# Kernel tuning notes

Hardware: AMD Instinct MI355X
Metric: run time of the kernel (lower is better)

Reference implementation:

```python
import jax, jax.numpy as jnp
import numpy as np

HEADS = 8

def _ape(f, c):
    # sinusoidal positional encoding, matches PositionalEncoding buffer pe[:f]
    pos = jnp.arange(f, dtype=jnp.float32)[:, None]                      # [f,1]
    div = jnp.exp(jnp.arange(0, c, 2, dtype=jnp.float32) * (-np.log(10000.0) / c))  # [c/2]
    pe = jnp.zeros((f, c), dtype=jnp.float32)
    pe = pe.at[:, 0::2].set(jnp.sin(pos * div))
    pe = pe.at[:, 1::2].set(jnp.cos(pos * div))
    return pe


def setup_inputs() -> dict:
    key = jax.random.key(0)
    ks = jax.random.split(key, 6)
    b, f, d, c = 2, 16, 4096, 320
    s = 1.0 / np.sqrt(c)
    return {
        'hidden_states': jax.random.normal(ks[0], (b * f, d, c), dtype=jnp.float32),
        'Wq': jax.random.normal(ks[1], (c, c), dtype=jnp.float32) * s,
        'Wk': jax.random.normal(ks[2], (c, c), dtype=jnp.float32) * s,
        'Wv': jax.random.normal(ks[3], (c, c), dtype=jnp.float32) * s,
        'Wo': jax.random.normal(ks[4], (c, c), dtype=jnp.float32) * s,
        'bo': jnp.zeros((c,), dtype=jnp.float32),
        'video_length': 16,
    }


def reference(hidden_states, Wq, Wk, Wv, Wo, bo, video_length):
    bf, d, c = hidden_states.shape
    f = video_length
    b = bf // f
    dh = c // HEADS
    # rearrange '(b f) d c -> (b d) f c'
    x = hidden_states.reshape(b, f, d, c).transpose(0, 2, 1, 3).reshape(b * d, f, c)
    # APE positional encoding over frames (dropout p=0)
    x = x + _ape(f, c)[None, :, :]
    # QKV projections (bias-free, diffusers CrossAttention)
    q = (x @ Wq.T).reshape(b * d, f, HEADS, dh)
    k = (x @ Wk.T).reshape(b * d, f, HEADS, dh)
    v = (x @ Wv.T).reshape(b * d, f, HEADS, dh)
    scale = dh ** -0.5
    scores = jnp.einsum('bqhd,bkhd->bhqk', q, k) * scale          # [B,h,f,f]
    causal = jnp.tril(jnp.ones((f, f), dtype=bool))
    scores = jnp.where(causal[None, None], scores, -jnp.inf)
    attn = jax.nn.softmax(scores, axis=-1)
    out = jnp.einsum('bhqk,bkhd->bqhd', attn, v).reshape(b * d, f, c)
    out = out @ Wo.T + bo
    # rearrange '(b d) f c -> (b f) d c'
    out = out.reshape(b, d, f, c).transpose(0, 2, 1, 3).reshape(b * f, d, c)
    return out
```

## Files before the change

kernel.cpp:

```cpp
#include <hip/hip_runtime.h>
#include <stdint.h>

#define F 16
#define CDIM 320
#define DDIM 4096
#define NSEQ 8192
#define WPB 4
#define THREADS 256
#define NT 20
#define KS 10

typedef __attribute__((ext_vector_type(8))) short short8;
typedef __attribute__((ext_vector_type(4))) float f32x4;

__device__ __forceinline__ unsigned short f2bf(float f) {
    union { float f; uint32_t u; } v; v.f = f;
    uint32_t r = v.u + 0x7FFFu + ((v.u >> 16) & 1u);
    return (unsigned short)(r >> 16);
}
__device__ __forceinline__ float bf2f(unsigned short h) {
    union { uint32_t u; float f; } v; v.u = ((uint32_t)h) << 16;
    return v.f;
}
__device__ __forceinline__ int swz(int row, int b) {
    return row * 640 + (b ^ ((row & 7) << 4));
}

__global__ __launch_bounds__(256)
void pack_weights_kernel(const float* __restrict__ Wq, const float* __restrict__ Wk,
                         const float* __restrict__ Wv, const float* __restrict__ Wo,
                         char* __restrict__ pk)
{
    const int t = blockIdx.x * 256 + threadIdx.x;
    if (t >= 4 * NT * KS * 64) return;
    const int lane = t & 63;
    const int rest = t >> 6;
    const int ks = rest % KS;
    const int nt = (rest / KS) % NT;
    const int m  = rest / (KS * NT);
    const float* W = (m == 0) ? Wq : (m == 1) ? Wk : (m == 2) ? Wv : Wo;
    const int g = lane >> 4, lr = lane & 15;
    const float* src = W + (size_t)(nt * 16 + lr) * CDIM + ks * 32 + g * 8;
    const f32x4 a = *(const f32x4*)src;
    const f32x4 b = *(const f32x4*)(src + 4);
    float vals[8] = {a[0], a[1], a[2], a[3], b[0], b[1], b[2], b[3]};
    short8 o;
#pragma unroll
    for (int j = 0; j < 8; ++j) o[j] = (short)f2bf(vals[j]);
    *(short8*)(pk + (size_t)t * 16) = o;
}

__global__ __launch_bounds__(THREADS, 2)
void temporal_attn_kernel(const float* __restrict__ hs,
                          const char* __restrict__ wpk,
                          const float* __restrict__ bo,
                          float* __restrict__ out)
{
    extern __shared__ __align__(16) char smem[];
    const int tid  = threadIdx.x;
    const int lane = tid & 63;
    const int wave = tid >> 6;
    const int g    = lane >> 4;
    const int lr   = lane & 15;

    const int seq = blockIdx.x * WPB + wave;
    const int bi  = seq >> 12;
    const int di  = seq & (DDIM - 1);

    char* const kbuf = smem + wave * 20480;
    char* const vbuf = kbuf + 10240;
    const char* const wl = wpk + lane * 16;

    const float* xrow = hs + ((size_t)(bi * F + lr) * DDIM + di) * CDIM;
    short8 axk[KS];
#pragma unroll
    for (int ks = 0; ks < KS; ++ks) {
        const int k0 = ks * 32 + g * 8;
        const f32x4 a = __builtin_nontemporal_load((const f32x4*)(xrow + k0));
        const f32x4 b = __builtin_nontemporal_load((const f32x4*)(xrow + k0 + 4));
        float xv[8] = {a[0], a[1], a[2], a[3], b[0], b[1], b[2], b[3]};
#pragma unroll
        for (int jj = 0; jj < 4; ++jj) {
            const float c0 = (float)(k0 + 2 * jj);
            const float dv = __expf(c0 * -0.028782313662425575f);
            const float ang = (float)lr * dv;
            xv[2 * jj]     += __sinf(ang);
            xv[2 * jj + 1] += __cosf(ang);
        }
        short8 t;
#pragma unroll
        for (int j = 0; j < 8; ++j) t[j] = (short)f2bf(xv[j]);
        axk[ks] = t;
    }

    auto proj = [&](int m, char* dst) {
        const char* base = wl + (size_t)(m * NT) * KS * 1024;
        short8 fa[KS], fb[KS];
#pragma unroll
        for (int ks = 0; ks < KS; ++ks)
            fa[ks] = *(const short8*)(base + (size_t)ks * 1024);
#pragma unroll 1
        for (int np = 0; np < 10; ++np) {
#pragma unroll
            for (int ks = 0; ks < KS; ++ks)
                fb[ks] = *(const short8*)(base + (size_t)((2 * np + 1) * KS + ks) * 1024);
            f32x4 a0 = {0.f, 0.f, 0.f, 0.f};
#pragma unroll
            for (int ks = 0; ks < KS; ++ks)
                a0 = __builtin_amdgcn_mfma_f32_16x16x32_bf16(axk[ks], fa[ks], a0, 0, 0, 0);
            if (np < 9) {
#pragma unroll
                for (int ks = 0; ks < KS; ++ks)
                    fa[ks] = *(const short8*)(base + (size_t)((2 * np + 2) * KS + ks) * 1024);
            }
            f32x4 a1 = {0.f, 0.f, 0.f, 0.f};
#pragma unroll
            for (int ks = 0; ks < KS; ++ks)
                a1 = __builtin_amdgcn_mfma_f32_16x16x32_bf16(axk[ks], fb[ks], a1, 0, 0, 0);
#pragma unroll
            for (int r = 0; r < 4; ++r) {
                const int row = g * 4 + r;
                *(short*)(dst + swz(row, (2 * np * 16 + lr) * 2))       = (short)f2bf(a0[r]);
                *(short*)(dst + swz(row, ((2 * np + 1) * 16 + lr) * 2)) = (short)f2bf(a1[r]);
            }
        }
    };

    proj(0, kbuf);
    short8 qreg[2][5];
#pragma unroll
    for (int h2 = 0; h2 < 2; ++h2)
#pragma unroll
        for (int j5 = 0; j5 < 5; ++j5)
            qreg[h2][j5] = *(const short8*)(kbuf + swz(lr, (g + 4 * h2) * 80 + j5 * 16));
    proj(1, kbuf);
    proj(2, vbuf);

    const float scale = 0.15811388300841897f;
#pragma unroll
    for (int h2 = 0; h2 < 2; ++h2) {
        const int cb = (g + 4 * h2) * 80;
        float s[F];
#pragma unroll
        for (int kk = 0; kk < F; ++kk) s[kk] = 0.f;
#pragma unroll
        for (int j5 = 0; j5 < 5; ++j5) {
            float qf[8];
#pragma unroll
            for (int j = 0; j < 8; ++j) qf[j] = bf2f((unsigned short)qreg[h2][j5][j]);
#pragma unroll
            for (int kk = 0; kk < F; ++kk) {
                short8 k8 = *(const short8*)(kbuf + swz(kk, cb + j5 * 16));
#pragma unroll
                for (int j = 0; j < 8; ++j) s[kk] += qf[j] * bf2f((unsigned short)k8[j]);
            }
        }
        float m = -1e30f;
#pragma unroll
        for (int kk = 0; kk < F; ++kk) {
            s[kk] = (kk <= lr) ? s[kk] * scale : -1e30f;
            m = fmaxf(m, s[kk]);
        }
        float sum = 0.f;
#pragma unroll
        for (int kk = 0; kk < F; ++kk) { s[kk] = __expf(s[kk] - m); sum += s[kk]; }
        const float inv = 1.f / sum;
#pragma unroll
        for (int kk = 0; kk < F; ++kk) s[kk] *= inv;

#pragma unroll
        for (int j5 = 0; j5 < 5; ++j5) {
            float a8[8];
#pragma unroll
            for (int j = 0; j < 8; ++j) a8[j] = 0.f;
#pragma unroll
            for (int kk = 0; kk < F; ++kk) {
                short8 v8 = *(const short8*)(vbuf + swz(kk, cb + j5 * 16));
#pragma unroll
                for (int j = 0; j < 8; ++j) a8[j] += s[kk] * bf2f((unsigned short)v8[j]);
            }
            short8 t;
#pragma unroll
            for (int j = 0; j < 8; ++j) t[j] = (short)f2bf(a8[j]);
            *(short8*)(kbuf + swz(lr, cb + j5 * 16)) = t;
        }
    }

    short8 aof[KS];
#pragma unroll
    for (int ks = 0; ks < KS; ++ks)
        aof[ks] = *(const short8*)(kbuf + swz(lr, ks * 64 + g * 16));

    {
        const char* base = wl + (size_t)(3 * NT) * KS * 1024;
        short8 fa[KS], fb[KS];
#pragma unroll
        for (int ks = 0; ks < KS; ++ks)
            fa[ks] = *(const short8*)(base + (size_t)ks * 1024);
#pragma unroll 1
        for (int np = 0; np < 10; ++np) {
#pragma unroll
            for (int ks = 0; ks < KS; ++ks)
                fb[ks] = *(const short8*)(base + (size_t)((2 * np + 1) * KS + ks) * 1024);
            f32x4 a0 = {0.f, 0.f, 0.f, 0.f};
#pragma unroll
            for (int ks = 0; ks < KS; ++ks)
                a0 = __builtin_amdgcn_mfma_f32_16x16x32_bf16(aof[ks], fa[ks], a0, 0, 0, 0);
            if (np < 9) {
#pragma unroll
                for (int ks = 0; ks < KS; ++ks)
                    fa[ks] = *(const short8*)(base + (size_t)((2 * np + 2) * KS + ks) * 1024);
            }
            f32x4 a1 = {0.f, 0.f, 0.f, 0.f};
#pragma unroll
            for (int ks = 0; ks < KS; ++ks)
                a1 = __builtin_amdgcn_mfma_f32_16x16x32_bf16(aof[ks], fb[ks], a1, 0, 0, 0);

            const int c0 = 2 * np * 16 + lr;
            const int c1 = c0 + 16;
            const float bias0 = bo[c0];
            const float bias1 = bo[c1];
#pragma unroll
            for (int r = 0; r < 4; ++r) {
                float* rowp = out + ((size_t)(bi * F + g * 4 + r) * DDIM + di) * CDIM;
                rowp[c0] = a0[r] + bias0;
                rowp[c1] = a1[r] + bias1;
            }
        }
    }
}

extern "C" void kernel_launch(void* const* d_in, const int* in_sizes, int n_in,
                              void* d_out, int out_size, void* d_ws, size_t ws_size,
                              hipStream_t stream) {
    const float* hs = (const float*)d_in[0];
    const float* Wq = (const float*)d_in[1];
    const float* Wk = (const float*)d_in[2];
    const float* Wv = (const float*)d_in[3];
    const float* Wo = (const float*)d_in[4];
    const float* bo = (const float*)d_in[5];
    float* out = (float*)d_out;
    char* wpk = (char*)d_ws;

    pack_weights_kernel<<<dim3((4 * NT * KS * 64 + 255) / 256), dim3(256), 0, stream>>>(
        Wq, Wk, Wv, Wo, wpk);

    const int lds = WPB * 20480;
    (void)hipFuncSetAttribute((const void*)temporal_attn_kernel,
                              hipFuncAttributeMaxDynamicSharedMemorySize, lds);
    temporal_attn_kernel<<<dim3(NSEQ / WPB), dim3(THREADS), lds, stream>>>(
        hs, wpk, bo, out);
}
```

Baseline: 275.4 us.

## Process heads in two halves to shrink LDS footprint per wave

Restructures the Q/K/V projections and attention to run per half of the heads (4 heads at a time), reusing one 6 KB LDS buffer per half instead of 20 KB K/V buffers per wave. The Q fragment registers shrink, and the output-projection input is gathered from the two half buffers. Waves per block also drop from 4 to 2. The aim is lower LDS use and register pressure so more waves fit per CU. In exchange there are more block launches and the weight loads are split into smaller loops.

Measured after the change: 721.9 us. 162% more time.

```diff
diff --git a/kernel.cpp b/kernel.cpp
--- a/kernel.cpp
+++ b/kernel.cpp
@@ -5,10 +5,11 @@
 #define CDIM 320
 #define DDIM 4096
 #define NSEQ 8192
-#define WPB 4
-#define THREADS 256
+#define WPB 2
+#define THREADS (WPB*64)
 #define NT 20
 #define KS 10
+#define HBUF 6144
 
 typedef __attribute__((ext_vector_type(8))) short short8;
 typedef __attribute__((ext_vector_type(4))) float f32x4;
@@ -22,8 +23,8 @@
     union { uint32_t u; float f; } v; v.u = ((uint32_t)h) << 16;
     return v.f;
 }
-__device__ __forceinline__ int swz(int row, int b) {
-    return row * 640 + (b ^ ((row & 7) << 4));
+__device__ __forceinline__ int hswz(int row, int b) {
+    return row * 384 + (b ^ ((row & 7) << 4));
 }
 
 __global__ __launch_bounds__(256)
@@ -67,8 +68,8 @@
     const int bi  = seq >> 12;
     const int di  = seq & (DDIM - 1);
 
-    char* const kbuf = smem + wave * 20480;
-    char* const vbuf = kbuf + 10240;
+    char* const X0 = smem + wave * (2 * HBUF);
+    char* const X1 = X0 + HBUF;
     const char* const wl = wpk + lane * 16;
 
     const float* xrow = hs + ((size_t)(bi * F + lr) * DDIM + di) * CDIM;
@@ -93,14 +94,14 @@
         axk[ks] = t;
     }
 
-    auto proj = [&](int m, char* dst) {
-        const char* base = wl + (size_t)(m * NT) * KS * 1024;
+    auto projh = [&](int m, int h2, char* dst) {
+        const char* base = wl + (size_t)((m * NT + h2 * 10) * KS) * 1024;
         short8 fa[KS], fb[KS];
 #pragma unroll
         for (int ks = 0; ks < KS; ++ks)
             fa[ks] = *(const short8*)(base + (size_t)ks * 1024);
 #pragma unroll 1
-        for (int np = 0; np < 10; ++np) {
+        for (int np = 0; np < 5; ++np) {
 #pragma unroll
             for (int ks = 0; ks < KS; ++ks)
                 fb[ks] = *(const short8*)(base + (size_t)((2 * np + 1) * KS + ks) * 1024);
@@ -108,7 +109,7 @@
 #pragma unroll
             for (int ks = 0; ks < KS; ++ks)
                 a0 = __builtin_amdgcn_mfma_f32_16x16x32_bf16(axk[ks], fa[ks], a0, 0, 0, 0);
-            if (np < 9) {
+            if (np < 4) {
 #pragma unroll
                 for (int ks = 0; ks < KS; ++ks)
                     fa[ks] = *(const short8*)(base + (size_t)((2 * np + 2) * KS + ks) * 1024);
@@ -120,26 +121,27 @@
 #pragma unroll
             for (int r = 0; r < 4; ++r) {
                 const int row = g * 4 + r;
-                *(short*)(dst + swz(row, (2 * np * 16 + lr) * 2))       = (short)f2bf(a0[r]);
-                *(short*)(dst + swz(row, ((2 * np + 1) * 16 + lr) * 2)) = (short)f2bf(a1[r]);
+                *(short*)(dst + hswz(row, 64 * np + 2 * lr))      = (short)f2bf(a0[r]);
+                *(short*)(dst + hswz(row, 64 * np + 32 + 2 * lr)) = (short)f2bf(a1[r]);
             }
         }
     };
 
-    proj(0, kbuf);
-    short8 qreg[2][5];
-#pragma unroll
-    for (int h2 = 0; h2 < 2; ++h2)
+    const float scale = 0.15811388300841897f;
+    const int cb = g * 80;
+
+#pragma unroll 1
+    for (int h2 = 0; h2 < 2; ++h2) {
+        char* const X = h2 ? X1 : X0;
+
+        projh(0, h2, X);
+        short8 qp[5];
 #pragma unroll
         for (int j5 = 0; j5 < 5; ++j5)
-            qreg[h2][j5] = *(const short8*)(kbuf + swz(lr, (g + 4 * h2) * 80 + j5 * 16));
-    proj(1, kbuf);
-    proj(2, vbuf);
-
-    const float scale = 0.15811388300841897f;
-#pragma unroll
-    for (int h2 = 0; h2 < 2; ++h2) {
-        const int cb = (g + 4 * h2) * 80;
+            qp[j5] = *(const short8*)(X + hswz(lr, cb + j5 * 16));
+
+        projh(1, h2, X);
+
         float s[F];
 #pragma unroll
         for (int kk = 0; kk < F; ++kk) s[kk] = 0.f;
@@ -147,10 +149,10 @@
         for (int j5 = 0; j5 < 5; ++j5) {
             float qf[8];
 #pragma unroll
-            for (int j = 0; j < 8; ++j) qf[j] = bf2f((unsigned short)qreg[h2][j5][j]);
+            for (int j = 0; j < 8; ++j) qf[j] = bf2f((unsigned short)qp[j5][j]);
 #pragma unroll
             for (int kk = 0; kk < F; ++kk) {
-                short8 k8 = *(const short8*)(kbuf + swz(kk, cb + j5 * 16));
+                short8 k8 = *(const short8*)(X + hswz(kk, cb + j5 * 16));
 #pragma unroll
                 for (int j = 0; j < 8; ++j) s[kk] += qf[j] * bf2f((unsigned short)k8[j]);
             }
@@ -168,6 +170,8 @@
 #pragma unroll
         for (int kk = 0; kk < F; ++kk) s[kk] *= inv;
 
+        projh(2, h2, X);
+
 #pragma unroll
         for (int j5 = 0; j5 < 5; ++j5) {
             float a8[8];
@@ -175,21 +179,24 @@
             for (int j = 0; j < 8; ++j) a8[j] = 0.f;
 #pragma unroll
             for (int kk = 0; kk < F; ++kk) {
-                short8 v8 = *(const short8*)(vbuf + swz(kk, cb + j5 * 16));
+                short8 v8 = *(const short8*)(X + hswz(kk, cb + j5 * 16));
 #pragma unroll
                 for (int j = 0; j < 8; ++j) a8[j] += s[kk] * bf2f((unsigned short)v8[j]);
             }
             short8 t;
 #pragma unroll
             for (int j = 0; j < 8; ++j) t[j] = (short)f2bf(a8[j]);
-            *(short8*)(kbuf + swz(lr, cb + j5 * 16)) = t;
+            *(short8*)(X + hswz(lr, cb + j5 * 16)) = t;
         }
     }
 
     short8 aof[KS];
 #pragma unroll
-    for (int ks = 0; ks < KS; ++ks)
-        aof[ks] = *(const short8*)(kbuf + swz(lr, ks * 64 + g * 16));
+    for (int ks = 0; ks < KS; ++ks) {
+        const char* Xh = (ks < 5) ? X0 : X1;
+        const int chunk = ks * 4 + g - 20 * (ks / 5);
+        aof[ks] = *(const short8*)(Xh + hswz(lr, chunk * 16));
+    }
 
     {
         const char* base = wl + (size_t)(3 * NT) * KS * 1024;
@@ -245,7 +252,7 @@
     pack_weights_kernel<<<dim3((4 * NT * KS * 64 + 255) / 256), dim3(256), 0, stream>>>(
         Wq, Wk, Wv, Wo, wpk);
 
-    const int lds = WPB * 20480;
+    const int lds = WPB * 2 * HBUF;
     (void)hipFuncSetAttribute((const void*)temporal_attn_kernel,
                               hipFuncAttributeMaxDynamicSharedMemorySize, lds);
     temporal_attn_kernel<<<dim3(NSEQ / WPB), dim3(THREADS), lds, stream>>>(
```
